# Kernel tuning notes

Hardware: AMD Instinct MI355X
Metric: run time of the kernel (lower is better)

Reference implementation:

```python
import jax, jax.numpy as jnp
import numpy as np

H = 2048  # hidden_size
I = 8192  # intermediate_size
B, S = 4, 2048


def setup_inputs() -> dict:
    key = jax.random.key(0)
    ks = jax.random.split(key, 8)
    scale = 1.0 / np.sqrt(H)
    scale_i = 1.0 / np.sqrt(I)
    x = jax.random.normal(ks[0], (B, S, H), dtype=jnp.float32)
    mask = jax.random.randint(ks[1], (B, S), 0, 2) > 0  # bool per-token routing
    # torch nn.Linear weights are [out_features, in_features]
    w1 = jax.random.normal(ks[2], (I, H), dtype=jnp.float32) * scale
    w2 = jax.random.normal(ks[3], (H, I), dtype=jnp.float32) * scale_i
    w3 = jax.random.normal(ks[4], (I, H), dtype=jnp.float32) * scale
    u1 = jax.random.normal(ks[5], (I, H), dtype=jnp.float32) * scale
    u2 = jax.random.normal(ks[6], (H, I), dtype=jnp.float32) * scale_i
    u3 = jax.random.normal(ks[7], (I, H), dtype=jnp.float32) * scale
    return {"x": x, "mask": mask, "w1": w1, "w2": w2, "w3": w3,
            "u1": u1, "u2": u2, "u3": u3}


def reference(x, mask, w1, w2, w3, u1, u2, u3):
    # branch 1 SwiGLU: silu(x @ w1^T) * (x @ w3^T), then w2
    proj1 = jax.nn.silu(jnp.einsum('bsh,ih->bsi', x, w1)) * jnp.einsum('bsh,ih->bsi', x, w3)
    proj2 = jax.nn.silu(jnp.einsum('bsh,ih->bsi', x, u1)) * jnp.einsum('bsh,ih->bsi', x, u3)
    out1 = jnp.einsum('bsi,hi->bsh', proj1, w2)
    out2 = jnp.einsum('bsi,hi->bsh', proj2, u2)
    m = mask[:, :, None]
    return jnp.where(m, out1, out2)
```

## Files before the change

### kernel.cpp

```cpp
#include <hip/hip_runtime.h>
#include <hip/hip_bf16.h>
#include <stdint.h>

#define DIM_H 2048
#define DIM_I 8192
#define TOKENS 8192
#define RB256 34
#define CROWS (RB256*256)

typedef __attribute__((ext_vector_type(8))) short bf16x8;
typedef __attribute__((ext_vector_type(4))) float f32x4;

#define MF(a,b,c) __builtin_amdgcn_mfma_f32_16x16x32_bf16((a),(b),(c),0,0,0)

__device__ __forceinline__ unsigned short f2bf(float f) {
    union { float f; unsigned u; } v; v.f = f;
    return (unsigned short)((v.u + 0x7FFF + ((v.u >> 16) & 1)) >> 16);
}

__global__ __launch_bounds__(256) void cvt_kernel(const float* __restrict__ in,
                                                  unsigned short* __restrict__ out,
                                                  int n4) {
    int stride = gridDim.x * blockDim.x;
    for (int j = blockIdx.x * blockDim.x + threadIdx.x; j < n4; j += stride) {
        float4 v = reinterpret_cast<const float4*>(in)[j];
        ushort4 o;
        o.x = f2bf(v.x); o.y = f2bf(v.y); o.z = f2bf(v.z); o.w = f2bf(v.w);
        reinterpret_cast<ushort4*>(out)[j] = o;
    }
}

__global__ __launch_bounds__(256) void cvt13_kernel(const float* __restrict__ w1,
                                                    const float* __restrict__ w3,
                                                    unsigned short* __restrict__ W13,
                                                    int n4) {
    int stride = gridDim.x * blockDim.x;
    for (int j = blockIdx.x * blockDim.x + threadIdx.x; j < n4; j += stride) {
        int flat = j << 2;
        int R = flat >> 11;
        int col = flat & 2047;
        int orow = ((R >> 4) << 5) | (R & 15);
        float4 v1 = reinterpret_cast<const float4*>(w1)[j];
        float4 v3 = reinterpret_cast<const float4*>(w3)[j];
        ushort4 o1, o3;
        o1.x=f2bf(v1.x); o1.y=f2bf(v1.y); o1.z=f2bf(v1.z); o1.w=f2bf(v1.w);
        o3.x=f2bf(v3.x); o3.y=f2bf(v3.y); o3.z=f2bf(v3.z); o3.w=f2bf(v3.w);
        *reinterpret_cast<ushort4*>(&W13[(size_t)orow * DIM_H + col]) = o1;
        *reinterpret_cast<ushort4*>(&W13[(size_t)(orow + 16) * DIM_H + col]) = o3;
    }
}

__global__ __launch_bounds__(256) void compact_kernel(const int* __restrict__ mask,
                                                      int* __restrict__ idx,
                                                      int* __restrict__ hdr) {
    __shared__ int cnt[256];
    const int t = threadIdx.x;
    const int base = t * 32;
    unsigned bits = 0;
#pragma unroll
    for (int j = 0; j < 32; ++j)
        if (mask[base + j] != 0) bits |= (1u << j);
    const int c = __popc(bits);
    cnt[t] = c;
    __syncthreads();
    for (int off = 1; off < 256; off <<= 1) {
        int v = cnt[t];
        int add = (t >= off) ? cnt[t - off] : 0;
        __syncthreads();
        cnt[t] = v + add;
        __syncthreads();
    }
    const int Mw  = cnt[255];
    const int MwP = (Mw + 255) & ~255;
    const int Mu  = TOKENS - Mw;
    const int MuP = (Mu + 255) & ~255;

    for (int j = t; j < CROWS; j += 256) idx[j] = -1;
    __syncthreads();

    int pw = cnt[t] - c;
    int pz = base - pw;
#pragma unroll
    for (int j = 0; j < 32; ++j) {
        int tok = base + j;
        if ((bits >> j) & 1) idx[pw++] = tok;
        else                 idx[MwP + pz++] = tok;
    }
    if (t == 0) {
        hdr[0] = MwP >> 8;
        hdr[1] = (MwP + MuP) >> 8;
        hdr[2] = Mw;
        hdr[3] = Mu;
    }
}


#define LDF4(D0,D1,D2,D3, SB, RB) do { \
    const unsigned short* _sl = &smem[(SB)]; \
    D0 = *reinterpret_cast<const bf16x8*>(&_sl[((RB) +  0)*32 + c16r]); \
    D1 = *reinterpret_cast<const bf16x8*>(&_sl[((RB) + 16)*32 + c16r]); \
    D2 = *reinterpret_cast<const bf16x8*>(&_sl[((RB) + 32)*32 + c16r]); \
    D3 = *reinterpret_cast<const bf16x8*>(&_sl[((RB) + 48)*32 + c16r]); \
} while(0)

#define STAGE2(UB_, S0_, S1_, KOFS_) do { \
    __builtin_amdgcn_global_load_lds((const __attribute__((address_space(1))) void*)((S0_) + (KOFS_)), \
        (__attribute__((address_space(3))) void*)&smem[(UB_) + wave*512], 16, 0, 0); \
    __builtin_amdgcn_global_load_lds((const __attribute__((address_space(1))) void*)((S1_) + (KOFS_)), \
        (__attribute__((address_space(3))) void*)&smem[(UB_) + 4096 + wave*512], 16, 0, 0); \
} while(0)

#define STAGE1(UB_, S0_, KOFS_) \
    __builtin_amdgcn_global_load_lds((const __attribute__((address_space(1))) void*)((S0_) + (KOFS_)), \
        (__attribute__((address_space(3))) void*)&smem[(UB_) + wave*512], 16, 0, 0)

#define MFMA32_G1() do { \
  acc[0][0]=MF(af0,bfr0,acc[0][0]); acc[0][1]=MF(af0,bfr1,acc[0][1]); acc[0][2]=MF(af0,bfr2,acc[0][2]); acc[0][3]=MF(af0,bfr3,acc[0][3]); \
  acc[1][0]=MF(af1,bfr0,acc[1][0]); acc[1][1]=MF(af1,bfr1,acc[1][1]); acc[1][2]=MF(af1,bfr2,acc[1][2]); acc[1][3]=MF(af1,bfr3,acc[1][3]); \
  acc[2][0]=MF(af2,bfr0,acc[2][0]); acc[2][1]=MF(af2,bfr1,acc[2][1]); acc[2][2]=MF(af2,bfr2,acc[2][2]); acc[2][3]=MF(af2,bfr3,acc[2][3]); \
  acc[3][0]=MF(af3,bfr0,acc[3][0]); acc[3][1]=MF(af3,bfr1,acc[3][1]); acc[3][2]=MF(af3,bfr2,acc[3][2]); acc[3][3]=MF(af3,bfr3,acc[3][3]); \
  acc[4][0]=MF(af4,bfr0,acc[4][0]); acc[4][1]=MF(af4,bfr1,acc[4][1]); acc[4][2]=MF(af4,bfr2,acc[4][2]); acc[4][3]=MF(af4,bfr3,acc[4][3]); \
  acc[5][0]=MF(af5,bfr0,acc[5][0]); acc[5][1]=MF(af5,bfr1,acc[5][1]); acc[5][2]=MF(af5,bfr2,acc[5][2]); acc[5][3]=MF(af5,bfr3,acc[5][3]); \
  acc[6][0]=MF(af6,bfr0,acc[6][0]); acc[6][1]=MF(af6,bfr1,acc[6][1]); acc[6][2]=MF(af6,bfr2,acc[6][2]); acc[6][3]=MF(af6,bfr3,acc[6][3]); \
  acc[7][0]=MF(af7,bfr0,acc[7][0]); acc[7][1]=MF(af7,bfr1,acc[7][1]); acc[7][2]=MF(af7,bfr2,acc[7][2]); acc[7][3]=MF(af7,bfr3,acc[7][3]); \
} while(0)

__global__ __launch_bounds__(512, 2) void gemm1_kernel(
    const unsigned short* __restrict__ xb,
    const unsigned short* __restrict__ W13,
    const unsigned short* __restrict__ U13,
    const int* __restrict__ idx, const int* __restrict__ hdr,
    unsigned short* __restrict__ P)
{
    __shared__ __align__(16) unsigned short smem[65536];
    const int wB  = hdr[0];
    const int rbT = hdr[1];
    const int nwg = gridDim.x;
    const int q8  = nwg >> 3;
    const int swz = ((int)blockIdx.x & 7) * q8 + ((int)blockIdx.x >> 3);
    const int rb = swz % RB256;
    const int bx = swz / RB256;
    if (rb >= rbT) return;
    const unsigned short* Bm = (rb < wB) ? W13 : U13;
    const int bm0 = rb << 8;
    const int bn0 = bx << 8;

    const int tid  = threadIdx.x;
    const int lane = tid & 63;
    const int wave = tid >> 6;
    const int wrM = wave >> 2;
    const int wcN = wave & 3;
    const int rAb = wrM * 128 + (lane & 15);
    const int rBb = wcN * 64 + (lane & 15);
    const int c16r = (((lane >> 4) ^ ((lane >> 1) & 3))) << 3;

    const int p0 = tid, p1 = 512 + tid;
    const int r0 = p0 >> 2, r1 = p1 >> 2;
    const int c0 = ((p0 & 3) ^ ((r0 >> 1) & 3)) << 3;
    const int c1 = ((p1 & 3) ^ ((r1 >> 1) & 3)) << 3;
    int t0 = idx[bm0 + r0]; if (t0 < 0) t0 = 0;
    int t1 = idx[bm0 + r1]; if (t1 < 0) t1 = 0;
    const unsigned short* sa0 = xb + (size_t)t0 * DIM_H + c0;
    const unsigned short* sa1 = xb + (size_t)t1 * DIM_H + c1;
    const unsigned short* sb0 = Bm + (size_t)(bn0 + r0) * DIM_H + c0;
    const unsigned short* sb1 = Bm + (size_t)(bn0 + r1) * DIM_H + c1;

    f32x4 acc[8][4] = {};
    bf16x8 af0, af1, af2, af3, af4, af5, af6, af7, bfr0, bfr1, bfr2, bfr3;

    STAGE2(0,     sa0, sa1, 0);
    STAGE2(16384, sb0, sb1, 0);
    STAGE2(8192,  sa0, sa1, 32);
    STAGE2(24576, sb0, sb1, 32);
    STAGE2(32768, sa0, sa1, 64);
    STAGE2(49152, sb0, sb1, 64);
    asm volatile("s_waitcnt vmcnt(8)" ::: "memory");
    __builtin_amdgcn_s_barrier();
    int ko = 96;
    for (int t = 0; t < 32; ++t) {
        const int cur = (t & 1) << 15;
        const int nxt = cur ^ 32768;
        LDF4(af0,af1,af2,af3, cur,          rAb);
        LDF4(af4,af5,af6,af7, cur,          rAb + 64);
        LDF4(bfr0,bfr1,bfr2,bfr3, cur + 16384, rBb);
        STAGE2(nxt + 8192,  sa0, sa1, ko);
        STAGE2(nxt + 24576, sb0, sb1, ko);
        __builtin_amdgcn_s_setprio(1);
        MFMA32_G1();
        __builtin_amdgcn_s_setprio(0);
        asm volatile("s_waitcnt vmcnt(8)" ::: "memory");
        __builtin_amdgcn_s_barrier();
        LDF4(af0,af1,af2,af3, cur + 8192,   rAb);
        LDF4(af4,af5,af6,af7, cur + 8192,   rAb + 64);
        LDF4(bfr0,bfr1,bfr2,bfr3, cur + 24576, rBb);
        STAGE2(cur,         sa0, sa1, ko + 32);
        STAGE2(cur + 16384, sb0, sb1, ko + 32);
        ko += 64;
        __builtin_amdgcn_s_setprio(1);
        MFMA32_G1();
        __builtin_amdgcn_s_setprio(0);
        asm volatile("s_waitcnt vmcnt(8)" ::: "memory");
        __builtin_amdgcn_s_barrier();
    }

    const int crow = (lane >> 4) << 2;
    const int ccol = lane & 15;
    unsigned short* Pw = P + (size_t)(bm0 + wrM * 128) * DIM_I
                           + (size_t)bx * 128 + wcN * 32 + ccol;
#pragma unroll
    for (int m = 0; m < 8; ++m) {
#pragma unroll
        for (int q = 0; q < 2; ++q) {
            f32x4 h1 = acc[m][2 * q];
            f32x4 h3 = acc[m][2 * q + 1];
#pragma unroll
            for (int r = 0; r < 4; ++r) {
                float a = h1[r];
                float p = a * (1.0f / (1.0f + __expf(-a))) * h3[r];
                Pw[(size_t)(m * 16 + crow + r) * DIM_I + q * 16] = f2bf(p);
            }
        }
    }
}

#define MFMA16Q(AF0,AF1,AF2,AF3, B0,B1,B2,B3) do { \
  acc[0][0]=MF(AF0,B0,acc[0][0]); acc[0][1]=MF(AF0,B1,acc[0][1]); acc[0][2]=MF(AF0,B2,acc[0][2]); acc[0][3]=MF(AF0,B3,acc[0][3]); \
  acc[1][0]=MF(AF1,B0,acc[1][0]); acc[1][1]=MF(AF1,B1,acc[1][1]); acc[1][2]=MF(AF1,B2,acc[1][2]); acc[1][3]=MF(AF1,B3,acc[1][3]); \
  acc[2][0]=MF(AF2,B0,acc[2][0]); acc[2][1]=MF(AF2,B1,acc[2][1]); acc[2][2]=MF(AF2,B2,acc[2][2]); acc[2][3]=MF(AF2,B3,acc[2][3]); \
  acc[3][0]=MF(AF3,B0,acc[3][0]); acc[3][1]=MF(AF3,B1,acc[3][1]); acc[3][2]=MF(AF3,B2,acc[3][2]); acc[3][3]=MF(AF3,B3,acc[3][3]); \
} while(0)

__global__ __launch_bounds__(512, 2) void gemm2_kernel(
    const unsigned short* __restrict__ P,
    const unsigned short* __restrict__ w2b, const unsigned short* __restrict__ u2b,
    const int* __restrict__ idx, const int* __restrict__ hdr,
    float* __restrict__ out)
{
    __shared__ __align__(16) unsigned short smem[73728];
    const int wB2  = hdr[0] * 2;
    const int rbT2 = hdr[1] * 2;
    const int nwg = gridDim.x;
    const int q8  = nwg >> 3;
    const int swz = ((int)blockIdx.x & 7) * q8 + ((int)blockIdx.x >> 3);
    const int rb = swz % 68;
    const int bx = swz / 68;
    if (rb >= rbT2) return;
    const unsigned short* Bm = (rb < wB2) ? w2b : u2b;
    const int bm0 = rb << 7;
    const int bn0 = bx << 8;

    const int tid  = threadIdx.x;
    const int lane = tid & 63;
    const int wave = tid >> 6;
    const int wrM = wave >> 2;
    const int wcN = wave & 3;
    const int rAb = wrM * 64 + (lane & 15);
    const int rBb = wcN * 64 + (lane & 15);
    const int c16r = (((lane >> 4) ^ ((lane >> 1) & 3))) << 3;

    const int r0 = tid >> 2, r1 = 128 + r0;
    const int c0 = ((tid & 3) ^ ((r0 >> 1) & 3)) << 3;
    const int c1 = ((tid & 3) ^ ((r1 >> 1) & 3)) << 3;
    const unsigned short* sa0 = P  + (size_t)(bm0 + r0) * DIM_I + c0;
    const unsigned short* sb0 = Bm + (size_t)(bn0 + r0) * DIM_I + c0;
    const unsigned short* sb1 = Bm + (size_t)(bn0 + r1) * DIM_I + c1;

    f32x4 acc[4][4] = {};
    bf16x8 af0, af1, af2, af3, af4, af5, af6, af7;
    bf16x8 bfr0, bfr1, bfr2, bfr3, bfr4, bfr5, bfr6, bfr7;

    STAGE1(0,     sa0, 0);
    STAGE1(4096,  sa0, 32);
    STAGE2(8192,  sb0, sb1, 0);
    STAGE2(16384, sb0, sb1, 32);
    STAGE1(24576,         sa0, 64);
    STAGE1(24576 + 4096,  sa0, 96);
    STAGE2(24576 + 8192,  sb0, sb1, 64);
    STAGE2(24576 + 16384, sb0, sb1, 96);
    asm volatile("s_waitcnt vmcnt(6)" ::: "memory");
    __builtin_amdgcn_s_barrier();
    int ko = 128, cb = 0;
    for (int t = 0; t < 128; ++t) {
        const int base = cb * 24576;
        int nb = base + 49152; if (nb >= 73728) nb -= 73728;
        LDF4(af0,af1,af2,af3,     base,          rAb);
        LDF4(af4,af5,af6,af7,     base + 4096,   rAb);
        LDF4(bfr0,bfr1,bfr2,bfr3, base + 8192,   rBb);
        LDF4(bfr4,bfr5,bfr6,bfr7, base + 16384,  rBb);
        STAGE1(nb,         sa0, ko);
        STAGE1(nb + 4096,  sa0, ko + 32);
        STAGE2(nb + 8192,  sb0, sb1, ko);
        STAGE2(nb + 16384, sb0, sb1, ko + 32);
        ko += 64;
        __builtin_amdgcn_s_setprio(1);
        MFMA16Q(af0,af1,af2,af3, bfr0,bfr1,bfr2,bfr3);
        MFMA16Q(af4,af5,af6,af7, bfr4,bfr5,bfr6,bfr7);
        __builtin_amdgcn_s_setprio(0);
        asm volatile("s_waitcnt vmcnt(6)" ::: "memory");
        __builtin_amdgcn_s_barrier();
        cb = (cb == 2) ? 0 : cb + 1;
    }

    const int crow = (lane >> 4) << 2;
    const int ccol = lane & 15;
#pragma unroll
    for (int m = 0; m < 4; ++m) {
#pragma unroll
        for (int r = 0; r < 4; ++r) {
            int rowc = bm0 + wrM * 64 + m * 16 + crow + r;
            int g = idx[rowc];
            if (g >= 0) {
                float* op = out + (size_t)g * DIM_H + bn0 + wcN * 64 + ccol;
#pragma unroll
                for (int n = 0; n < 4; ++n) op[n * 16] = acc[m][n][r];
            }
        }
    }
}

extern "C" void kernel_launch(void* const* d_in, const int* in_sizes, int n_in,
                              void* d_out, int out_size, void* d_ws, size_t ws_size,
                              hipStream_t stream) {
    const float* x    = (const float*)d_in[0];
    const int*   mask = (const int*)d_in[1];
    const float* w1 = (const float*)d_in[2];
    const float* w2 = (const float*)d_in[3];
    const float* w3 = (const float*)d_in[4];
    const float* u1 = (const float*)d_in[5];
    const float* u2 = (const float*)d_in[6];
    const float* u3 = (const float*)d_in[7];
    float* out = (float*)d_out;

    const size_t XN   = (size_t)TOKENS * DIM_H;
    const size_t WN   = (size_t)DIM_I * DIM_H;
    const size_t PN   = (size_t)CROWS * DIM_I;
    const size_t W13N = 2 * WN;

    unsigned short* ws  = (unsigned short*)d_ws;
    unsigned short* xb  = ws;
    unsigned short* Pb  = xb + XN;
    unsigned short* W13 = Pb + PN;
    unsigned short* U13 = W13 + W13N;
    int* idx = (int*)(U13 + W13N);
    int* hdr = idx + CROWS;
    unsigned short* w2b = W13;
    unsigned short* u2b = U13;

    const int cvtBlocks = 2048;
    const int n4 = (int)(WN / 4);

    cvt_kernel  <<<cvtBlocks, 256, 0, stream>>>(x, xb, (int)(XN / 4));
    cvt13_kernel<<<cvtBlocks, 256, 0, stream>>>(w1, w3, W13, n4);
    cvt13_kernel<<<cvtBlocks, 256, 0, stream>>>(u1, u3, U13, n4);
    compact_kernel<<<1, 256, 0, stream>>>(mask, idx, hdr);

    gemm1_kernel<<<64 * RB256, 512, 0, stream>>>(xb, W13, U13, idx, hdr, Pb);

    cvt_kernel<<<cvtBlocks, 256, 0, stream>>>(w2, w2b, n4);
    cvt_kernel<<<cvtBlocks, 256, 0, stream>>>(u2, u2b, n4);

    gemm2_kernel<<<8 * 68, 512, 0, stream>>>(Pb, w2b, u2b, idx, hdr, out);
}
```

Measured before the change: 1.056 ms.

## Switch both GEMMs to 32x32x16 MFMA with software-pipelined LDS fragment reads

Replaces the 16x16x32 bf16 MFMA tiles in both GEMM kernels with 32x32x16 MFMA, which gives larger accumulator tiles per instruction and fewer LDS fragment reads per FLOP. The W1/W3 interleave is changed to 32-row groups so the gate and up halves line up with the new accumulator layout. The K loop is restructured to double-buffer register fragments, loading the next half-K fragments while the current MFMAs run. Epilogues are rewritten for the 32x32 output layout, which produces a different store pattern and could raise register pressure.

```diff
diff --git a/kernel.cpp b/kernel.cpp
--- a/kernel.cpp
+++ b/kernel.cpp
@@ -9,9 +9,9 @@
 #define CROWS (RB256*256)
 
 typedef __attribute__((ext_vector_type(8))) short bf16x8;
-typedef __attribute__((ext_vector_type(4))) float f32x4;
-
-#define MF(a,b,c) __builtin_amdgcn_mfma_f32_16x16x32_bf16((a),(b),(c),0,0,0)
+typedef __attribute__((ext_vector_type(16))) float f32x16;
+
+#define MF32(a,b,c) __builtin_amdgcn_mfma_f32_32x32x16_bf16((a),(b),(c),0,0,0)
 
 __device__ __forceinline__ unsigned short f2bf(float f) {
     union { float f; unsigned u; } v; v.f = f;
@@ -39,14 +39,14 @@
         int flat = j << 2;
         int R = flat >> 11;
         int col = flat & 2047;
-        int orow = ((R >> 4) << 5) | (R & 15);
+        int orow = ((R >> 5) << 6) | (R & 31);
         float4 v1 = reinterpret_cast<const float4*>(w1)[j];
         float4 v3 = reinterpret_cast<const float4*>(w3)[j];
         ushort4 o1, o3;
         o1.x=f2bf(v1.x); o1.y=f2bf(v1.y); o1.z=f2bf(v1.z); o1.w=f2bf(v1.w);
         o3.x=f2bf(v3.x); o3.y=f2bf(v3.y); o3.z=f2bf(v3.z); o3.w=f2bf(v3.w);
         *reinterpret_cast<ushort4*>(&W13[(size_t)orow * DIM_H + col]) = o1;
-        *reinterpret_cast<ushort4*>(&W13[(size_t)(orow + 16) * DIM_H + col]) = o3;
+        *reinterpret_cast<ushort4*>(&W13[(size_t)(orow + 32) * DIM_H + col]) = o3;
     }
 }
 
@@ -95,14 +95,6 @@
 }
 
 
-#define LDF4(D0,D1,D2,D3, SB, RB) do { \
-    const unsigned short* _sl = &smem[(SB)]; \
-    D0 = *reinterpret_cast<const bf16x8*>(&_sl[((RB) +  0)*32 + c16r]); \
-    D1 = *reinterpret_cast<const bf16x8*>(&_sl[((RB) + 16)*32 + c16r]); \
-    D2 = *reinterpret_cast<const bf16x8*>(&_sl[((RB) + 32)*32 + c16r]); \
-    D3 = *reinterpret_cast<const bf16x8*>(&_sl[((RB) + 48)*32 + c16r]); \
-} while(0)
-
 #define STAGE2(UB_, S0_, S1_, KOFS_) do { \
     __builtin_amdgcn_global_load_lds((const __attribute__((address_space(1))) void*)((S0_) + (KOFS_)), \
         (__attribute__((address_space(3))) void*)&smem[(UB_) + wave*512], 16, 0, 0); \
@@ -114,15 +106,25 @@
     __builtin_amdgcn_global_load_lds((const __attribute__((address_space(1))) void*)((S0_) + (KOFS_)), \
         (__attribute__((address_space(3))) void*)&smem[(UB_) + wave*512], 16, 0, 0)
 
-#define MFMA32_G1() do { \
-  acc[0][0]=MF(af0,bfr0,acc[0][0]); acc[0][1]=MF(af0,bfr1,acc[0][1]); acc[0][2]=MF(af0,bfr2,acc[0][2]); acc[0][3]=MF(af0,bfr3,acc[0][3]); \
-  acc[1][0]=MF(af1,bfr0,acc[1][0]); acc[1][1]=MF(af1,bfr1,acc[1][1]); acc[1][2]=MF(af1,bfr2,acc[1][2]); acc[1][3]=MF(af1,bfr3,acc[1][3]); \
-  acc[2][0]=MF(af2,bfr0,acc[2][0]); acc[2][1]=MF(af2,bfr1,acc[2][1]); acc[2][2]=MF(af2,bfr2,acc[2][2]); acc[2][3]=MF(af2,bfr3,acc[2][3]); \
-  acc[3][0]=MF(af3,bfr0,acc[3][0]); acc[3][1]=MF(af3,bfr1,acc[3][1]); acc[3][2]=MF(af3,bfr2,acc[3][2]); acc[3][3]=MF(af3,bfr3,acc[3][3]); \
-  acc[4][0]=MF(af4,bfr0,acc[4][0]); acc[4][1]=MF(af4,bfr1,acc[4][1]); acc[4][2]=MF(af4,bfr2,acc[4][2]); acc[4][3]=MF(af4,bfr3,acc[4][3]); \
-  acc[5][0]=MF(af5,bfr0,acc[5][0]); acc[5][1]=MF(af5,bfr1,acc[5][1]); acc[5][2]=MF(af5,bfr2,acc[5][2]); acc[5][3]=MF(af5,bfr3,acc[5][3]); \
-  acc[6][0]=MF(af6,bfr0,acc[6][0]); acc[6][1]=MF(af6,bfr1,acc[6][1]); acc[6][2]=MF(af6,bfr2,acc[6][2]); acc[6][3]=MF(af6,bfr3,acc[6][3]); \
-  acc[7][0]=MF(af7,bfr0,acc[7][0]); acc[7][1]=MF(af7,bfr1,acc[7][1]); acc[7][2]=MF(af7,bfr2,acc[7][2]); acc[7][3]=MF(af7,bfr3,acc[7][3]); \
+#define RD(V, EO) V = *reinterpret_cast<const bf16x8*>(&smem[(EO)])
+
+#define G1_RDA(V0,V1,V2,V3, SB, OFF) do { \
+    RD(V0, (SB) + wrM*4096 +    0 + (OFF)); \
+    RD(V1, (SB) + wrM*4096 + 1024 + (OFF)); \
+    RD(V2, (SB) + wrM*4096 + 2048 + (OFF)); \
+    RD(V3, (SB) + wrM*4096 + 3072 + (OFF)); \
+} while(0)
+#define G1_RDB(V0,V1, SB, OFF) do { \
+    RD(V0, (SB) + wcN*2048 +    0 + (OFF)); \
+    RD(V1, (SB) + wcN*2048 + 1024 + (OFF)); \
+} while(0)
+#define G1_MFMA(A0,A1,A2,A3,B0,B1) do { \
+    __builtin_amdgcn_s_setprio(1); \
+    acc00=MF32(A0,B0,acc00); acc01=MF32(A0,B1,acc01); \
+    acc10=MF32(A1,B0,acc10); acc11=MF32(A1,B1,acc11); \
+    acc20=MF32(A2,B0,acc20); acc21=MF32(A2,B1,acc21); \
+    acc30=MF32(A3,B0,acc30); acc31=MF32(A3,B1,acc31); \
+    __builtin_amdgcn_s_setprio(0); \
 } while(0)
 
 __global__ __launch_bounds__(512, 2) void gemm1_kernel(
@@ -137,9 +139,9 @@
     const int rbT = hdr[1];
     const int nwg = gridDim.x;
     const int q8  = nwg >> 3;
-    const int swz = ((int)blockIdx.x & 7) * q8 + ((int)blockIdx.x >> 3);
-    const int rb = swz % RB256;
-    const int bx = swz / RB256;
+    const int swzb = ((int)blockIdx.x & 7) * q8 + ((int)blockIdx.x >> 3);
+    const int rb = swzb % RB256;
+    const int bx = swzb / RB256;
     if (rb >= rbT) return;
     const unsigned short* Bm = (rb < wB) ? W13 : U13;
     const int bm0 = rb << 8;
@@ -150,14 +152,14 @@
     const int wave = tid >> 6;
     const int wrM = wave >> 2;
     const int wcN = wave & 3;
-    const int rAb = wrM * 128 + (lane & 15);
-    const int rBb = wcN * 64 + (lane & 15);
-    const int c16r = (((lane >> 4) ^ ((lane >> 1) & 3))) << 3;
-
-    const int p0 = tid, p1 = 512 + tid;
-    const int r0 = p0 >> 2, r1 = p1 >> 2;
-    const int c0 = ((p0 & 3) ^ ((r0 >> 1) & 3)) << 3;
-    const int c1 = ((p1 & 3) ^ ((r1 >> 1) & 3)) << 3;
+    const int kh   = lane >> 5;
+    const int swz  = (lane >> 1) & 3;
+    const int off0 = (lane & 31) * 32 + ((kh ^ swz) << 3);
+    const int off1 = (lane & 31) * 32 + (((2 + kh) ^ swz) << 3);
+
+    const int r0 = tid >> 2, r1 = 128 + r0;
+    const int c0 = ((tid & 3) ^ ((r0 >> 1) & 3)) << 3;
+    const int c1 = ((tid & 3) ^ ((r1 >> 1) & 3)) << 3;
     int t0 = idx[bm0 + r0]; if (t0 < 0) t0 = 0;
     int t1 = idx[bm0 + r1]; if (t1 < 0) t1 = 0;
     const unsigned short* sa0 = xb + (size_t)t0 * DIM_H + c0;
@@ -165,8 +167,10 @@
     const unsigned short* sb0 = Bm + (size_t)(bn0 + r0) * DIM_H + c0;
     const unsigned short* sb1 = Bm + (size_t)(bn0 + r1) * DIM_H + c1;
 
-    f32x4 acc[8][4] = {};
-    bf16x8 af0, af1, af2, af3, af4, af5, af6, af7, bfr0, bfr1, bfr2, bfr3;
+    f32x16 acc00 = {}, acc01 = {}, acc10 = {}, acc11 = {};
+    f32x16 acc20 = {}, acc21 = {}, acc30 = {}, acc31 = {};
+    bf16x8 xa0, xa1, xa2, xa3, xb0, xb1;
+    bf16x8 ya0, ya1, ya2, ya3, yb0, yb1;
 
     STAGE2(0,     sa0, sa1, 0);
     STAGE2(16384, sb0, sb1, 0);
@@ -176,58 +180,66 @@
     STAGE2(49152, sb0, sb1, 64);
     asm volatile("s_waitcnt vmcnt(8)" ::: "memory");
     __builtin_amdgcn_s_barrier();
-    int ko = 96;
+    G1_RDA(xa0,xa1,xa2,xa3, 0,     off0);
+    G1_RDB(xb0,xb1,        16384,  off0);
+    int ko2 = 96, ko6 = 128;
     for (int t = 0; t < 32; ++t) {
         const int cur = (t & 1) << 15;
         const int nxt = cur ^ 32768;
-        LDF4(af0,af1,af2,af3, cur,          rAb);
-        LDF4(af4,af5,af6,af7, cur,          rAb + 64);
-        LDF4(bfr0,bfr1,bfr2,bfr3, cur + 16384, rBb);
-        STAGE2(nxt + 8192,  sa0, sa1, ko);
-        STAGE2(nxt + 24576, sb0, sb1, ko);
-        __builtin_amdgcn_s_setprio(1);
-        MFMA32_G1();
-        __builtin_amdgcn_s_setprio(0);
+        G1_RDA(ya0,ya1,ya2,ya3, cur,         off1);
+        G1_RDB(yb0,yb1,         cur + 16384, off1);
+        STAGE2(nxt + 8192,  sa0, sa1, ko2);
+        STAGE2(nxt + 24576, sb0, sb1, ko2);
+        G1_MFMA(xa0,xa1,xa2,xa3, xb0,xb1);
         asm volatile("s_waitcnt vmcnt(8)" ::: "memory");
         __builtin_amdgcn_s_barrier();
-        LDF4(af0,af1,af2,af3, cur + 8192,   rAb);
-        LDF4(af4,af5,af6,af7, cur + 8192,   rAb + 64);
-        LDF4(bfr0,bfr1,bfr2,bfr3, cur + 24576, rBb);
-        STAGE2(cur,         sa0, sa1, ko + 32);
-        STAGE2(cur + 16384, sb0, sb1, ko + 32);
-        ko += 64;
-        __builtin_amdgcn_s_setprio(1);
-        MFMA32_G1();
-        __builtin_amdgcn_s_setprio(0);
+        G1_RDA(xa0,xa1,xa2,xa3, cur + 8192,  off0);
+        G1_RDB(xb0,xb1,         cur + 24576, off0);
+        STAGE2(cur,         sa0, sa1, ko6);
+        STAGE2(cur + 16384, sb0, sb1, ko6);
+        G1_MFMA(ya0,ya1,ya2,ya3, yb0,yb1);
+        G1_RDA(ya0,ya1,ya2,ya3, cur + 8192,  off1);
+        G1_RDB(yb0,yb1,         cur + 24576, off1);
+        G1_MFMA(xa0,xa1,xa2,xa3, xb0,xb1);
         asm volatile("s_waitcnt vmcnt(8)" ::: "memory");
         __builtin_amdgcn_s_barrier();
-    }
-
-    const int crow = (lane >> 4) << 2;
-    const int ccol = lane & 15;
+        G1_RDA(xa0,xa1,xa2,xa3, nxt,         off0);
+        G1_RDB(xb0,xb1,         nxt + 16384, off0);
+        G1_MFMA(ya0,ya1,ya2,ya3, yb0,yb1);
+        ko2 += 64; ko6 += 64;
+    }
+
+    const int kh4 = kh << 2;
     unsigned short* Pw = P + (size_t)(bm0 + wrM * 128) * DIM_I
-                           + (size_t)bx * 128 + wcN * 32 + ccol;
-#pragma unroll
-    for (int m = 0; m < 8; ++m) {
-#pragma unroll
-        for (int q = 0; q < 2; ++q) {
-            f32x4 h1 = acc[m][2 * q];
-            f32x4 h3 = acc[m][2 * q + 1];
-#pragma unroll
-            for (int r = 0; r < 4; ++r) {
-                float a = h1[r];
-                float p = a * (1.0f / (1.0f + __expf(-a))) * h3[r];
-                Pw[(size_t)(m * 16 + crow + r) * DIM_I + q * 16] = f2bf(p);
-            }
-        }
-    }
-}
-
-#define MFMA16Q(AF0,AF1,AF2,AF3, B0,B1,B2,B3) do { \
-  acc[0][0]=MF(AF0,B0,acc[0][0]); acc[0][1]=MF(AF0,B1,acc[0][1]); acc[0][2]=MF(AF0,B2,acc[0][2]); acc[0][3]=MF(AF0,B3,acc[0][3]); \
-  acc[1][0]=MF(AF1,B0,acc[1][0]); acc[1][1]=MF(AF1,B1,acc[1][1]); acc[1][2]=MF(AF1,B2,acc[1][2]); acc[1][3]=MF(AF1,B3,acc[1][3]); \
-  acc[2][0]=MF(AF2,B0,acc[2][0]); acc[2][1]=MF(AF2,B1,acc[2][1]); acc[2][2]=MF(AF2,B2,acc[2][2]); acc[2][3]=MF(AF2,B3,acc[2][3]); \
-  acc[3][0]=MF(AF3,B0,acc[3][0]); acc[3][1]=MF(AF3,B1,acc[3][1]); acc[3][2]=MF(AF3,B2,acc[3][2]); acc[3][3]=MF(AF3,B3,acc[3][3]); \
+                           + (size_t)bx * 128 + wcN * 32 + (lane & 31);
+#define G1EPI(H1, H3, M) do { \
+    _Pragma("unroll") \
+    for (int reg = 0; reg < 16; ++reg) { \
+        float a = H1[reg]; \
+        float p = a * (1.0f / (1.0f + __expf(-a))) * H3[reg]; \
+        int rr = (reg & 3) + ((reg >> 2) << 3) + kh4; \
+        Pw[(size_t)((M) * 32 + rr) * DIM_I] = f2bf(p); \
+    } } while(0)
+    G1EPI(acc00, acc01, 0);
+    G1EPI(acc10, acc11, 1);
+    G1EPI(acc20, acc21, 2);
+    G1EPI(acc30, acc31, 3);
+#undef G1EPI
+}
+
+#define G2_RDA(V0,V1, SB, OFF) do { \
+    RD(V0, (SB) + wrM*2048 +    0 + (OFF)); \
+    RD(V1, (SB) + wrM*2048 + 1024 + (OFF)); \
+} while(0)
+#define G2_RDB(V0,V1, SB, OFF) do { \
+    RD(V0, (SB) + wcN*2048 +    0 + (OFF)); \
+    RD(V1, (SB) + wcN*2048 + 1024 + (OFF)); \
+} while(0)
+#define G2_MFMA(A0,A1,B0,B1) do { \
+    __builtin_amdgcn_s_setprio(1); \
+    acc00=MF32(A0,B0,acc00); acc01=MF32(A0,B1,acc01); \
+    acc10=MF32(A1,B0,acc10); acc11=MF32(A1,B1,acc11); \
+    __builtin_amdgcn_s_setprio(0); \
 } while(0)
 
 __global__ __launch_bounds__(512, 2) void gemm2_kernel(
@@ -241,9 +253,9 @@
     const int rbT2 = hdr[1] * 2;
     const int nwg = gridDim.x;
     const int q8  = nwg >> 3;
-    const int swz = ((int)blockIdx.x & 7) * q8 + ((int)blockIdx.x >> 3);
-    const int rb = swz % 68;
-    const int bx = swz / 68;
+    const int swzb = ((int)blockIdx.x & 7) * q8 + ((int)blockIdx.x >> 3);
+    const int rb = swzb % 68;
+    const int bx = swzb / 68;
     if (rb >= rbT2) return;
     const unsigned short* Bm = (rb < wB2) ? w2b : u2b;
     const int bm0 = rb << 7;
@@ -254,9 +266,10 @@
     const int wave = tid >> 6;
     const int wrM = wave >> 2;
     const int wcN = wave & 3;
-    const int rAb = wrM * 64 + (lane & 15);
-    const int rBb = wcN * 64 + (lane & 15);
-    const int c16r = (((lane >> 4) ^ ((lane >> 1) & 3))) << 3;
+    const int kh   = lane >> 5;
+    const int swz  = (lane >> 1) & 3;
+    const int off0 = (lane & 31) * 32 + ((kh ^ swz) << 3);
+    const int off1 = (lane & 31) * 32 + (((2 + kh) ^ swz) << 3);
 
     const int r0 = tid >> 2, r1 = 128 + r0;
     const int c0 = ((tid & 3) ^ ((r0 >> 1) & 3)) << 3;
@@ -265,9 +278,8 @@
     const unsigned short* sb0 = Bm + (size_t)(bn0 + r0) * DIM_I + c0;
     const unsigned short* sb1 = Bm + (size_t)(bn0 + r1) * DIM_I + c1;
 
-    f32x4 acc[4][4] = {};
-    bf16x8 af0, af1, af2, af3, af4, af5, af6, af7;
-    bf16x8 bfr0, bfr1, bfr2, bfr3, bfr4, bfr5, bfr6, bfr7;
+    f32x16 acc00 = {}, acc01 = {}, acc10 = {}, acc11 = {};
+    bf16x8 xa0, xa1, xb0, xb1, ya0, ya1, yb0, yb1;
 
     STAGE1(0,     sa0, 0);
     STAGE1(4096,  sa0, 32);
@@ -279,43 +291,50 @@
     STAGE2(24576 + 16384, sb0, sb1, 96);
     asm volatile("s_waitcnt vmcnt(6)" ::: "memory");
     __builtin_amdgcn_s_barrier();
+    G2_RDA(xa0,xa1, 0,    off0);
+    G2_RDB(xb0,xb1, 8192, off0);
     int ko = 128, cb = 0;
     for (int t = 0; t < 128; ++t) {
         const int base = cb * 24576;
         int nb = base + 49152; if (nb >= 73728) nb -= 73728;
-        LDF4(af0,af1,af2,af3,     base,          rAb);
-        LDF4(af4,af5,af6,af7,     base + 4096,   rAb);
-        LDF4(bfr0,bfr1,bfr2,bfr3, base + 8192,   rBb);
-        LDF4(bfr4,bfr5,bfr6,bfr7, base + 16384,  rBb);
+        G2_RDA(ya0,ya1, base,        off1);
+        G2_RDB(yb0,yb1, base + 8192, off1);
         STAGE1(nb,         sa0, ko);
         STAGE1(nb + 4096,  sa0, ko + 32);
         STAGE2(nb + 8192,  sb0, sb1, ko);
         STAGE2(nb + 16384, sb0, sb1, ko + 32);
-        ko += 64;
-        __builtin_amdgcn_s_setprio(1);
-        MFMA16Q(af0,af1,af2,af3, bfr0,bfr1,bfr2,bfr3);
-        MFMA16Q(af4,af5,af6,af7, bfr4,bfr5,bfr6,bfr7);
-        __builtin_amdgcn_s_setprio(0);
+        G2_MFMA(xa0,xa1, xb0,xb1);
+        G2_RDA(xa0,xa1, base + 4096,  off0);
+        G2_RDB(xb0,xb1, base + 16384, off0);
+        G2_MFMA(ya0,ya1, yb0,yb1);
+        G2_RDA(ya0,ya1, base + 4096,  off1);
+        G2_RDB(yb0,yb1, base + 16384, off1);
+        G2_MFMA(xa0,xa1, xb0,xb1);
         asm volatile("s_waitcnt vmcnt(6)" ::: "memory");
         __builtin_amdgcn_s_barrier();
+        int b1 = base + 24576; if (b1 >= 73728) b1 -= 73728;
+        G2_RDA(xa0,xa1, b1,        off0);
+        G2_RDB(xb0,xb1, b1 + 8192, off0);
+        G2_MFMA(ya0,ya1, yb0,yb1);
+        ko += 64;
         cb = (cb == 2) ? 0 : cb + 1;
     }
 
-    const int crow = (lane >> 4) << 2;
-    const int ccol = lane & 15;
-#pragma unroll
-    for (int m = 0; m < 4; ++m) {
-#pragma unroll
-        for (int r = 0; r < 4; ++r) {
-            int rowc = bm0 + wrM * 64 + m * 16 + crow + r;
-            int g = idx[rowc];
-            if (g >= 0) {
-                float* op = out + (size_t)g * DIM_H + bn0 + wcN * 64 + ccol;
-#pragma unroll
-                for (int n = 0; n < 4; ++n) op[n * 16] = acc[m][n][r];
-            }
-        }
-    }
+    const int kh4 = kh << 2;
+    const int colb = bn0 + wcN * 64 + (lane & 31);
+#define G2EPI(ACC, M, N) do { \
+    _Pragma("unroll") \
+    for (int reg = 0; reg < 16; ++reg) { \
+        int rr = (reg & 3) + ((reg >> 2) << 3) + kh4; \
+        int rowc = bm0 + wrM * 64 + (M) * 32 + rr; \
+        int g = idx[rowc]; \
+        if (g >= 0) out[(size_t)g * DIM_H + colb + (N) * 32] = ACC[reg]; \
+    } } while(0)
+    G2EPI(acc00, 0, 0);
+    G2EPI(acc01, 0, 1);
+    G2EPI(acc10, 1, 0);
+    G2EPI(acc11, 1, 1);
+#undef G2EPI
 }
 
 extern "C" void kernel_launch(void* const* d_in, const int* in_sizes, int n_in,
```

Measured after the change: 1.124 ms. 1.06x slower.

## Double-buffer gemm1 LDS fragment registers to overlap LDS reads with MFMA

Applied to the files above, without the earlier changes.

gemm1 now keeps two register sets of A/B fragments. It loads the next k-slice from LDS into the spare set while the current set feeds the MFMAs, and the vmcnt wait is tightened from 8 to 4 so each stage is resident one step earlier. This is meant to hide LDS read latency behind matrix math. The cost is roughly double the fragment register count, which at 512 threads with 2 blocks per CU could cause spills or lower occupancy. In gemm2 the setprio calls move inside the MFMA macro, which brackets each half-group separately.

```diff
diff --git a/kernel.cpp b/kernel.cpp
--- a/kernel.cpp
+++ b/kernel.cpp
@@ -114,15 +114,17 @@
     __builtin_amdgcn_global_load_lds((const __attribute__((address_space(1))) void*)((S0_) + (KOFS_)), \
         (__attribute__((address_space(3))) void*)&smem[(UB_) + wave*512], 16, 0, 0)
 
-#define MFMA32_G1() do { \
-  acc[0][0]=MF(af0,bfr0,acc[0][0]); acc[0][1]=MF(af0,bfr1,acc[0][1]); acc[0][2]=MF(af0,bfr2,acc[0][2]); acc[0][3]=MF(af0,bfr3,acc[0][3]); \
-  acc[1][0]=MF(af1,bfr0,acc[1][0]); acc[1][1]=MF(af1,bfr1,acc[1][1]); acc[1][2]=MF(af1,bfr2,acc[1][2]); acc[1][3]=MF(af1,bfr3,acc[1][3]); \
-  acc[2][0]=MF(af2,bfr0,acc[2][0]); acc[2][1]=MF(af2,bfr1,acc[2][1]); acc[2][2]=MF(af2,bfr2,acc[2][2]); acc[2][3]=MF(af2,bfr3,acc[2][3]); \
-  acc[3][0]=MF(af3,bfr0,acc[3][0]); acc[3][1]=MF(af3,bfr1,acc[3][1]); acc[3][2]=MF(af3,bfr2,acc[3][2]); acc[3][3]=MF(af3,bfr3,acc[3][3]); \
-  acc[4][0]=MF(af4,bfr0,acc[4][0]); acc[4][1]=MF(af4,bfr1,acc[4][1]); acc[4][2]=MF(af4,bfr2,acc[4][2]); acc[4][3]=MF(af4,bfr3,acc[4][3]); \
-  acc[5][0]=MF(af5,bfr0,acc[5][0]); acc[5][1]=MF(af5,bfr1,acc[5][1]); acc[5][2]=MF(af5,bfr2,acc[5][2]); acc[5][3]=MF(af5,bfr3,acc[5][3]); \
-  acc[6][0]=MF(af6,bfr0,acc[6][0]); acc[6][1]=MF(af6,bfr1,acc[6][1]); acc[6][2]=MF(af6,bfr2,acc[6][2]); acc[6][3]=MF(af6,bfr3,acc[6][3]); \
-  acc[7][0]=MF(af7,bfr0,acc[7][0]); acc[7][1]=MF(af7,bfr1,acc[7][1]); acc[7][2]=MF(af7,bfr2,acc[7][2]); acc[7][3]=MF(af7,bfr3,acc[7][3]); \
+#define MFMA32_S(A0,A1,A2,A3,A4,A5,A6,A7,B0,B1,B2,B3) do { \
+  __builtin_amdgcn_s_setprio(1); \
+  acc[0][0]=MF(A0,B0,acc[0][0]); acc[0][1]=MF(A0,B1,acc[0][1]); acc[0][2]=MF(A0,B2,acc[0][2]); acc[0][3]=MF(A0,B3,acc[0][3]); \
+  acc[1][0]=MF(A1,B0,acc[1][0]); acc[1][1]=MF(A1,B1,acc[1][1]); acc[1][2]=MF(A1,B2,acc[1][2]); acc[1][3]=MF(A1,B3,acc[1][3]); \
+  acc[2][0]=MF(A2,B0,acc[2][0]); acc[2][1]=MF(A2,B1,acc[2][1]); acc[2][2]=MF(A2,B2,acc[2][2]); acc[2][3]=MF(A2,B3,acc[2][3]); \
+  acc[3][0]=MF(A3,B0,acc[3][0]); acc[3][1]=MF(A3,B1,acc[3][1]); acc[3][2]=MF(A3,B2,acc[3][2]); acc[3][3]=MF(A3,B3,acc[3][3]); \
+  acc[4][0]=MF(A4,B0,acc[4][0]); acc[4][1]=MF(A4,B1,acc[4][1]); acc[4][2]=MF(A4,B2,acc[4][2]); acc[4][3]=MF(A4,B3,acc[4][3]); \
+  acc[5][0]=MF(A5,B0,acc[5][0]); acc[5][1]=MF(A5,B1,acc[5][1]); acc[5][2]=MF(A5,B2,acc[5][2]); acc[5][3]=MF(A5,B3,acc[5][3]); \
+  acc[6][0]=MF(A6,B0,acc[6][0]); acc[6][1]=MF(A6,B1,acc[6][1]); acc[6][2]=MF(A6,B2,acc[6][2]); acc[6][3]=MF(A6,B3,acc[6][3]); \
+  acc[7][0]=MF(A7,B0,acc[7][0]); acc[7][1]=MF(A7,B1,acc[7][1]); acc[7][2]=MF(A7,B2,acc[7][2]); acc[7][3]=MF(A7,B3,acc[7][3]); \
+  __builtin_amdgcn_s_setprio(0); \
 } while(0)
 
 __global__ __launch_bounds__(512, 2) void gemm1_kernel(
@@ -137,9 +139,9 @@
     const int rbT = hdr[1];
     const int nwg = gridDim.x;
     const int q8  = nwg >> 3;
-    const int swz = ((int)blockIdx.x & 7) * q8 + ((int)blockIdx.x >> 3);
-    const int rb = swz % RB256;
-    const int bx = swz / RB256;
+    const int swzb = ((int)blockIdx.x & 7) * q8 + ((int)blockIdx.x >> 3);
+    const int rb = swzb % RB256;
+    const int bx = swzb / RB256;
     if (rb >= rbT) return;
     const unsigned short* Bm = (rb < wB) ? W13 : U13;
     const int bm0 = rb << 8;
@@ -166,40 +168,37 @@
     const unsigned short* sb1 = Bm + (size_t)(bn0 + r1) * DIM_H + c1;
 
     f32x4 acc[8][4] = {};
-    bf16x8 af0, af1, af2, af3, af4, af5, af6, af7, bfr0, bfr1, bfr2, bfr3;
-
-    STAGE2(0,     sa0, sa1, 0);
-    STAGE2(16384, sb0, sb1, 0);
-    STAGE2(8192,  sa0, sa1, 32);
-    STAGE2(24576, sb0, sb1, 32);
-    STAGE2(32768, sa0, sa1, 64);
-    STAGE2(49152, sb0, sb1, 64);
-    asm volatile("s_waitcnt vmcnt(8)" ::: "memory");
+    bf16x8 xa0,xa1,xa2,xa3,xa4,xa5,xa6,xa7, xb0,xb1,xb2,xb3;
+    bf16x8 ya0,ya1,ya2,ya3,ya4,ya5,ya6,ya7, yb0,yb1,yb2,yb3;
+
+    STAGE2(0,     sa0, sa1, 0);   STAGE2(16384, sb0, sb1, 0);
+    STAGE2(8192,  sa0, sa1, 32);  STAGE2(24576, sb0, sb1, 32);
+    STAGE2(32768, sa0, sa1, 64);  STAGE2(49152, sb0, sb1, 64);
+    asm volatile("s_waitcnt vmcnt(4)" ::: "memory");
     __builtin_amdgcn_s_barrier();
+    LDF4(xa0,xa1,xa2,xa3, 0, rAb);
+    LDF4(xa4,xa5,xa6,xa7, 0, rAb + 64);
+    LDF4(xb0,xb1,xb2,xb3, 16384, rBb);
     int ko = 96;
     for (int t = 0; t < 32; ++t) {
         const int cur = (t & 1) << 15;
         const int nxt = cur ^ 32768;
-        LDF4(af0,af1,af2,af3, cur,          rAb);
-        LDF4(af4,af5,af6,af7, cur,          rAb + 64);
-        LDF4(bfr0,bfr1,bfr2,bfr3, cur + 16384, rBb);
+        LDF4(ya0,ya1,ya2,ya3, cur + 8192,  rAb);
+        LDF4(ya4,ya5,ya6,ya7, cur + 8192,  rAb + 64);
+        LDF4(yb0,yb1,yb2,yb3, cur + 24576, rBb);
         STAGE2(nxt + 8192,  sa0, sa1, ko);
         STAGE2(nxt + 24576, sb0, sb1, ko);
-        __builtin_amdgcn_s_setprio(1);
-        MFMA32_G1();
-        __builtin_amdgcn_s_setprio(0);
-        asm volatile("s_waitcnt vmcnt(8)" ::: "memory");
+        MFMA32_S(xa0,xa1,xa2,xa3,xa4,xa5,xa6,xa7, xb0,xb1,xb2,xb3);
+        asm volatile("s_waitcnt vmcnt(4)" ::: "memory");
         __builtin_amdgcn_s_barrier();
-        LDF4(af0,af1,af2,af3, cur + 8192,   rAb);
-        LDF4(af4,af5,af6,af7, cur + 8192,   rAb + 64);
-        LDF4(bfr0,bfr1,bfr2,bfr3, cur + 24576, rBb);
+        LDF4(xa0,xa1,xa2,xa3, nxt,         rAb);
+        LDF4(xa4,xa5,xa6,xa7, nxt,         rAb + 64);
+        LDF4(xb0,xb1,xb2,xb3, nxt + 16384, rBb);
         STAGE2(cur,         sa0, sa1, ko + 32);
         STAGE2(cur + 16384, sb0, sb1, ko + 32);
         ko += 64;
-        __builtin_amdgcn_s_setprio(1);
-        MFMA32_G1();
-        __builtin_amdgcn_s_setprio(0);
-        asm volatile("s_waitcnt vmcnt(8)" ::: "memory");
+        MFMA32_S(ya0,ya1,ya2,ya3,ya4,ya5,ya6,ya7, yb0,yb1,yb2,yb3);
+        asm volatile("s_waitcnt vmcnt(4)" ::: "memory");
         __builtin_amdgcn_s_barrier();
     }
 
@@ -224,10 +223,12 @@
 }
 
 #define MFMA16Q(AF0,AF1,AF2,AF3, B0,B1,B2,B3) do { \
+  __builtin_amdgcn_s_setprio(1); \
   acc[0][0]=MF(AF0,B0,acc[0][0]); acc[0][1]=MF(AF0,B1,acc[0][1]); acc[0][2]=MF(AF0,B2,acc[0][2]); acc[0][3]=MF(AF0,B3,acc[0][3]); \
   acc[1][0]=MF(AF1,B0,acc[1][0]); acc[1][1]=MF(AF1,B1,acc[1][1]); acc[1][2]=MF(AF1,B2,acc[1][2]); acc[1][3]=MF(AF1,B3,acc[1][3]); \
   acc[2][0]=MF(AF2,B0,acc[2][0]); acc[2][1]=MF(AF2,B1,acc[2][1]); acc[2][2]=MF(AF2,B2,acc[2][2]); acc[2][3]=MF(AF2,B3,acc[2][3]); \
   acc[3][0]=MF(AF3,B0,acc[3][0]); acc[3][1]=MF(AF3,B1,acc[3][1]); acc[3][2]=MF(AF3,B2,acc[3][2]); acc[3][3]=MF(AF3,B3,acc[3][3]); \
+  __builtin_amdgcn_s_setprio(0); \
 } while(0)
 
 __global__ __launch_bounds__(512, 2) void gemm2_kernel(
@@ -292,10 +293,8 @@
         STAGE2(nb + 8192,  sb0, sb1, ko);
         STAGE2(nb + 16384, sb0, sb1, ko + 32);
         ko += 64;
-        __builtin_amdgcn_s_setprio(1);
         MFMA16Q(af0,af1,af2,af3, bfr0,bfr1,bfr2,bfr3);
         MFMA16Q(af4,af5,af6,af7, bfr4,bfr5,bfr6,bfr7);
-        __builtin_amdgcn_s_setprio(0);
         asm volatile("s_waitcnt vmcnt(6)" ::: "memory");
         __builtin_amdgcn_s_barrier();
         cb = (cb == 2) ? 0 : cb + 1;
```

After: 1.058 ms. No clear change (+0.2%).
